# Optimization experiments

Hardware: AMD Instinct MI355X
Metric: run time of the kernel (lower is better)

## Reference

```python
import jax, jax.numpy as jnp
import numpy as np

N_NODES, N_EDGES, BATCH = 50000, 100000, 256
H = 64            # dim_hidden_features
D_NODE, D_EDGE, D_RBF = 110, 8, 8
D_SET = 2 * H     # Set2Set input_dim = 128, output_dim = 256
D_HID = 512
D_CAT = 54
MP_STEPS, S2S_ITERS = 4, 3


def setup_inputs() -> dict:
    key = jax.random.key(0)
    ks = iter(jax.random.split(key, 48))

    def nrm(shape, s=0.05):
        return jax.random.normal(next(ks), shape, dtype=jnp.float32) * s

    inp = {}
    inp["node_attribute"] = jax.random.normal(next(ks), (N_NODES, D_NODE), dtype=jnp.float32)
    inp["edge_attribute"] = jax.random.normal(next(ks), (N_EDGES, D_EDGE), dtype=jnp.float32)
    inp["edge_length"] = jax.random.uniform(next(ks), (N_EDGES,), dtype=jnp.float32)
    inp["src"] = jax.random.randint(next(ks), (N_EDGES,), 0, N_NODES, dtype=jnp.int32)
    inp["dst"] = jax.random.randint(next(ks), (N_EDGES,), 0, N_NODES, dtype=jnp.int32)
    inp["node_graph"] = jnp.sort(jax.random.randint(next(ks), (N_NODES,), 0, BATCH, dtype=jnp.int32))
    # atom_feature_projector
    inp["proj_W"] = nrm((D_NODE, H)); inp["proj_b"] = jnp.zeros((H,), jnp.float32)
    # RBF layer: centers ~ U(0,1), beta = 10 (per reset_parameters)
    inp["centers"] = jax.random.uniform(next(ks), (D_RBF,), dtype=jnp.float32)
    inp["beta"] = jnp.full((D_RBF,), 10.0, jnp.float32)
    # NNConv edge function: Linear(16 -> 64*64), plus NNConv bias
    inp["bond_W"] = nrm((D_EDGE + D_RBF, H * H)); inp["bond_b"] = jnp.zeros((H * H,), jnp.float32)
    inp["conv_b"] = jnp.zeros((H,), jnp.float32)
    # GRU (input H, hidden H); PyTorch layout (3H, in)
    inp["gru_Wih"] = nrm((3 * H, H)); inp["gru_Whh"] = nrm((3 * H, H))
    inp["gru_bih"] = jnp.zeros((3 * H,), jnp.float32); inp["gru_bhh"] = jnp.zeros((3 * H,), jnp.float32)
    # Set2Set LSTM: input 2*D_SET=256, hidden D_SET=128, 2 layers; PyTorch layout (4H, in)
    inp["lstm_Wih0"] = nrm((4 * D_SET, 2 * D_SET)); inp["lstm_Whh0"] = nrm((4 * D_SET, D_SET))
    inp["lstm_bih0"] = jnp.zeros((4 * D_SET,), jnp.float32); inp["lstm_bhh0"] = jnp.zeros((4 * D_SET,), jnp.float32)
    inp["lstm_Wih1"] = nrm((4 * D_SET, D_SET)); inp["lstm_Whh1"] = nrm((4 * D_SET, D_SET))
    inp["lstm_bih1"] = jnp.zeros((4 * D_SET,), jnp.float32); inp["lstm_bhh1"] = jnp.zeros((4 * D_SET,), jnp.float32)
    # sparsify: Linear(256 -> 512) + PReLU(init 0.25)
    inp["sp_W"] = nrm((2 * D_SET, D_HID)); inp["sp_b"] = jnp.zeros((D_HID,), jnp.float32)
    inp["prelu_a"] = jnp.array([0.25], jnp.float32)
    # catalyst1 head: hiddens[0] (512->512 ReLU, 512->512 Tanh) then outputs[0] (512->54)
    inp["h0_W1"] = nrm((D_HID, D_HID)); inp["h0_b1"] = jnp.zeros((D_HID,), jnp.float32)
    inp["h0_W2"] = nrm((D_HID, D_HID)); inp["h0_b2"] = jnp.zeros((D_HID,), jnp.float32)
    inp["out_W"] = nrm((D_HID, D_CAT)); inp["out_b"] = jnp.zeros((D_CAT,), jnp.float32)
    return inp


def _lstm_cell(x, h, c, Wih, Whh, bih, bhh):
    # PyTorch LSTM gate order: i, f, g, o
    g = x @ Wih.T + bih + h @ Whh.T + bhh
    i, f, gg, o = jnp.split(g, 4, axis=-1)
    c = jax.nn.sigmoid(f) * c + jax.nn.sigmoid(i) * jnp.tanh(gg)
    h = jax.nn.sigmoid(o) * jnp.tanh(c)
    return h, c


def reference(node_attribute, edge_attribute, edge_length, src, dst, node_graph,
              proj_W, proj_b, centers, beta, bond_W, bond_b, conv_b,
              gru_Wih, gru_Whh, gru_bih, gru_bhh,
              lstm_Wih0, lstm_Whh0, lstm_bih0, lstm_bhh0,
              lstm_Wih1, lstm_Whh1, lstm_bih1, lstm_bhh1,
              sp_W, sp_b, prelu_a, h0_W1, h0_b1, h0_W2, h0_b2, out_W, out_b):
    n_nodes = node_attribute.shape[0]
    # atom feature projection
    x = jax.nn.relu(node_attribute @ proj_W + proj_b)                       # (N, H)
    # edge features = [edge_attribute, RBF(length)]
    rbf = jnp.exp(-beta * (edge_length[:, None] - centers[None, :]) ** 2)   # (E, 8)
    efeat = jnp.concatenate([edge_attribute, rbf], axis=-1)                 # (E, 16)
    # NNConv per-edge weight matrix; edge features are constant over MP steps
    W_e = (efeat @ bond_W + bond_b).reshape(-1, H, H)                       # (E, H, H)

    feat, h = x, x
    for _ in range(MP_STEPS):
        # NNConv: message = h_src @ W_e, sum-aggregated at dst, plus bias
        m = jnp.einsum('ei,eio->eo', feat[src], W_e)                        # (E, H)
        agg = jax.ops.segment_sum(m, dst, num_segments=n_nodes) + conv_b    # (N, H)
        gx = jax.nn.relu(agg)
        # GRU cell (PyTorch gate order r, z, n)
        gi = gx @ gru_Wih.T + gru_bih
        gh = h @ gru_Whh.T + gru_bhh
        i_r, i_z, i_n = jnp.split(gi, 3, axis=-1)
        h_r, h_z, h_n = jnp.split(gh, 3, axis=-1)
        r = jax.nn.sigmoid(i_r + h_r)
        z = jax.nn.sigmoid(i_z + h_z)
        n = jnp.tanh(i_n + r * h_n)
        h = (1.0 - z) * n + z * h
        feat = h
    node_agg = jnp.concatenate([feat, x], axis=-1)                          # (N, 2H)

    # Set2Set pooling over graphs (segment softmax attention, 2-layer LSTM)
    B = BATCH
    h0 = c0 = jnp.zeros((B, D_SET), node_agg.dtype)
    h1 = c1 = jnp.zeros((B, D_SET), node_agg.dtype)
    q_star = jnp.zeros((B, 2 * D_SET), node_agg.dtype)
    for _ in range(S2S_ITERS):
        h0, c0 = _lstm_cell(q_star, h0, c0, lstm_Wih0, lstm_Whh0, lstm_bih0, lstm_bhh0)
        h1, c1 = _lstm_cell(h0, h1, c1, lstm_Wih1, lstm_Whh1, lstm_bih1, lstm_bhh1)
        q = h1                                                              # (B, 128)
        e = jnp.sum(node_agg * q[node_graph], axis=-1)                      # (N,)
        emax = jax.ops.segment_max(e, node_graph, num_segments=B)
        p = jnp.exp(e - emax[node_graph])
        denom = jax.ops.segment_sum(p, node_graph, num_segments=B)
        alpha = p / denom[node_graph]                                       # per-graph softmax
        r_out = jax.ops.segment_sum(node_agg * alpha[:, None], node_graph, num_segments=B)
        q_star = jnp.concatenate([q, r_out], axis=-1)                       # (B, 256)

    # sparsify (Linear + PReLU)
    feats = q_star @ sp_W + sp_b                                            # (B, 512)
    feats = jnp.where(feats >= 0, feats, prelu_a * feats)
    # catalyst1 head
    hid = jnp.tanh(jax.nn.relu(feats @ h0_W1 + h0_b1) @ h0_W2 + h0_b2)
    return jax.nn.softmax(hid @ out_W + out_b, axis=-1)                     # (B, 54)
```

## Files before the change

### kernel.cpp

```cpp
#include <hip/hip_runtime.h>
#include <math.h>

constexpr int N = 50000;
constexpr int E = 100000;
constexpr int B = 256;
constexpr int H = 64;
constexpr int DN = 110;
constexpr int NBLK = (E + 63) / 64;

#define DEV __device__ __forceinline__

typedef __attribute__((ext_vector_type(8))) short short8;
typedef __attribute__((ext_vector_type(4))) float floatx4;

DEV float sigf(float x) { return 1.0f / (1.0f + expf(-x)); }

DEV short f2bf(float f) {
    unsigned u = __float_as_uint(f);
    unsigned r = (u + 0x7fffu + ((u >> 16) & 1u)) >> 16;
    return (short)r;
}
DEV float bf2f(short s) { return __uint_as_float(((unsigned)(unsigned short)s) << 16); }

DEV void cvt8(const float* p, short8& hi, short8& lo) {
    float4 u0 = *(const float4*)p;
    float4 u1 = *(const float4*)(p + 4);
    float vv[8] = {u0.x, u0.y, u0.z, u0.w, u1.x, u1.y, u1.z, u1.w};
#pragma unroll
    for (int j = 0; j < 8; ++j) {
        short hb = f2bf(vv[j]);
        hi[j] = hb;
        lo[j] = f2bf(vv[j] - bf2f(hb));
    }
}

__global__ void k_izero(int* p, int n) {
    int i = blockIdx.x * 256 + threadIdx.x;
    if (i < n) p[i] = 0;
}

DEV void d_transpose(const float* in, float* out, int R, int C, int idx) {
    int r = idx / C, c = idx % C;
    out[c * R + r] = in[idx];
}

DEV void d_prepB(const float* __restrict__ W, short* __restrict__ out,
                 int NT16, int ld, int trans, int ocap, int kcap, int idx) {
    int lane = idx & 63;
    int t = idx >> 6;
    int ntile = t % NT16;
    int kt = t / NT16;
    int quad = lane >> 4, col = lane & 15;
    int o = ntile * 16 + col;
    short hi[8], lo[8];
#pragma unroll
    for (int j = 0; j < 8; ++j) {
        int k = kt * 32 + quad * 8 + j;
        float v = 0.0f;
        if (o < ocap && k < kcap) v = trans ? W[(size_t)o * ld + k] : W[(size_t)k * ld + o];
        short hb = f2bf(v);
        hi[j] = hb;
        lo[j] = f2bf(v - bf2f(hb));
    }
    short* dh = out + (((size_t)(t * 2 + 0) * 64 + lane) * 8);
    short* dl = out + (((size_t)(t * 2 + 1) * 64 + lane) * 8);
#pragma unroll
    for (int j = 0; j < 8; ++j) { dh[j] = hi[j]; dl[j] = lo[j]; }
}

DEV void d_prepW(const float* __restrict__ bond_W, const float* __restrict__ bond_b,
                 short* __restrict__ wf, int idx) {
    int lane = idx & 63;
    int t = idx >> 6;
    int ks = t & 1;
    int nt = (t >> 1) & 3;
    int kk = t >> 3;
    const float* S = (kk < 16) ? (bond_W + kk * 4096) : bond_b;
    int quad = lane >> 4, col = lane & 15;
    short hi[8], lo[8];
#pragma unroll
    for (int j = 0; j < 8; ++j) {
        int i = ks * 32 + quad * 8 + j;
        float v = S[i * 64 + nt * 16 + col];
        short hb = f2bf(v);
        hi[j] = hb;
        lo[j] = f2bf(v - bf2f(hb));
    }
    short* dh = wf + (((size_t)(t * 2 + 0) * 64 + lane) * 8);
    short* dl = wf + (((size_t)(t * 2 + 1) * 64 + lane) * 8);
#pragma unroll
    for (int j = 0; j < 8; ++j) { dh[j] = hi[j]; dl[j] = lo[j]; }
}

__launch_bounds__(256)
__global__ void k_prep0(const float* lWih0, const float* lWhh0, const float* lWih1, const float* lWhh1,
                        float* lW0T, float* lU0T, float* lW1T, float* lU1T,
                        const float* bond_W, const float* bond_b, short* wf,
                        const float* gru_Wih, const float* gru_Whh, short* fgI, short* fgH,
                        const float* proj_W, short* fproj,
                        float* zreg) {
    int idx = blockIdx.x * 256 + threadIdx.x;
    if (idx < 131072) { d_transpose(lWih0, lW0T, 512, 256, idx); return; }
    idx -= 131072;
    if (idx < 65536) { d_transpose(lWhh0, lU0T, 512, 128, idx); return; }
    idx -= 65536;
    if (idx < 65536) { d_transpose(lWih1, lW1T, 512, 128, idx); return; }
    idx -= 65536;
    if (idx < 65536) { d_transpose(lWhh1, lU1T, 512, 128, idx); return; }
    idx -= 65536;
    if (idx < 8704) { d_prepW(bond_W, bond_b, wf, idx); return; }
    idx -= 8704;
    if (idx < 1536) { d_prepB(gru_Wih, fgI, 12, 64, 1, 192, 64, idx); return; }
    idx -= 1536;
    if (idx < 1536) { d_prepB(gru_Whh, fgH, 12, 64, 1, 192, 64, idx); return; }
    idx -= 1536;
    if (idx < 1024) { d_prepB(proj_W, fproj, 4, 64, 0, 64, DN, idx); return; }
    idx -= 1024;
    if (idx < 196608) { zreg[idx] = 0.0f; return; }
}
constexpr int PREP0_TOTAL = 131072 + 3 * 65536 + 8704 + 2 * 1536 + 1024 + 196608;

__launch_bounds__(256)
__global__ void k_prephead(const float* sp_W, short* fsp, const float* h0_W1, short* fw1,
                           const float* h0_W2, short* fw2, const float* out_W, short* fow) {
    int idx = blockIdx.x * 256 + threadIdx.x;
    if (idx < 16384) { d_prepB(sp_W, fsp, 32, 512, 0, 512, 256, idx); return; }
    idx -= 16384;
    if (idx < 32768) { d_prepB(h0_W1, fw1, 32, 512, 0, 512, 512, idx); return; }
    idx -= 32768;
    if (idx < 32768) { d_prepB(h0_W2, fw2, 32, 512, 0, 512, 512, idx); return; }
    idx -= 32768;
    if (idx < 4096) { d_prepB(out_W, fow, 4, 54, 0, 54, 512, idx); return; }
}
constexpr int PREPH_TOTAL = 16384 + 2 * 32768 + 4096;

__global__ void k_deg(const int* __restrict__ dst, int* __restrict__ deg) {
    int e = blockIdx.x * 256 + threadIdx.x;
    if (e < E) atomicAdd(&deg[dst[e]], 1);
}
__global__ void k_scan1(const int* __restrict__ deg, int* __restrict__ bsum) {
    __shared__ int s[256];
    int b = blockIdx.x, tid = threadIdx.x;
    int idx = b * 256 + tid;
    s[tid] = (idx < N) ? deg[idx] : 0;
    __syncthreads();
    for (int st = 128; st > 0; st >>= 1) {
        if (tid < st) s[tid] += s[tid + st];
        __syncthreads();
    }
    if (tid == 0) bsum[b] = s[0];
}
__global__ void k_scan2p(int* __restrict__ bsum, int nb) {
    __shared__ int s[256];
    int tid = threadIdx.x;
    int v = (tid < nb) ? bsum[tid] : 0;
    s[tid] = v;
    __syncthreads();
    for (int off = 1; off < 256; off <<= 1) {
        int t = (tid >= off) ? s[tid - off] : 0;
        __syncthreads();
        s[tid] += t;
        __syncthreads();
    }
    if (tid < nb) bsum[tid] = s[tid] - v;
}
__global__ void k_scan3(const int* __restrict__ deg, const int* __restrict__ bsum,
                        int* __restrict__ cursor, int* __restrict__ roff) {
    __shared__ int s[256];
    int b = blockIdx.x, tid = threadIdx.x;
    int idx = b * 256 + tid;
    int v = (idx < N) ? deg[idx] : 0;
    s[tid] = v;
    __syncthreads();
    for (int off = 1; off < 256; off <<= 1) {
        int t = (tid >= off) ? s[tid - off] : 0;
        __syncthreads();
        s[tid] += t;
        __syncthreads();
    }
    if (idx < N) {
        int start = bsum[b] + s[tid] - v;
        cursor[idx] = start;
        roff[idx] = start;
    }
    if (idx == 0) roff[N] = E;
}
__global__ void k_scat(const int* __restrict__ src, const int* __restrict__ dst,
                       int* __restrict__ cursor, int* __restrict__ srcp,
                       int* __restrict__ epos, int* __restrict__ dstp) {
    int e = blockIdx.x * 256 + threadIdx.x;
    if (e >= E) return;
    int d = dst[e];
    int pos = atomicAdd(&cursor[d], 1);
    srcp[pos] = src[e];
    dstp[pos] = d;
    epos[e] = pos;
}

__launch_bounds__(256)
__global__ void k_projm(const float* __restrict__ na, const short* __restrict__ fp,
                        const float* __restrict__ b, float* __restrict__ x,
                        short* __restrict__ hs) {
    __shared__ float as[16 * 132];
    int tid = threadIdx.x, lane = tid & 63, nt = tid >> 6;
    int quad = lane >> 4, col = lane & 15;
    int s0 = blockIdx.x * 16;
    for (int i = tid; i < 16 * DN; i += 256) {
        int r = i / DN, c = i % DN;
        as[r * 132 + c] = na[(size_t)s0 * DN + i];
    }
    for (int i = tid; i < 16 * 22; i += 256) {
        int r = i / 22, c = DN + i % 22;
        as[r * 132 + c] = 0.0f;
    }
    __syncthreads();
    const short8* F = (const short8*)fp;
    floatx4 T = {0.0f, 0.0f, 0.0f, 0.0f};
#pragma unroll
    for (int kt = 0; kt < 4; ++kt) {
        const float* ap = as + col * 132 + kt * 32 + quad * 8;
        short8 ah, al;
#pragma unroll
        for (int j = 0; j < 8; ++j) {
            float v = ap[j];
            short hb = f2bf(v);
            ah[j] = hb;
            al[j] = f2bf(v - bf2f(hb));
        }
        int t = kt * 4 + nt;
        short8 bh = F[(t * 2 + 0) * 64 + lane];
        short8 bl = F[(t * 2 + 1) * 64 + lane];
        T = __builtin_amdgcn_mfma_f32_16x16x32_bf16(ah, bh, T, 0, 0, 0);
        T = __builtin_amdgcn_mfma_f32_16x16x32_bf16(al, bh, T, 0, 0, 0);
        T = __builtin_amdgcn_mfma_f32_16x16x32_bf16(ah, bl, T, 0, 0, 0);
    }
    int o = nt * 16 + col;
    float bo = b[o];
#pragma unroll
    for (int r = 0; r < 4; ++r) {
        int n = s0 + quad * 4 + r;
        float v = fmaxf(T[r] + bo, 0.0f);
        x[(size_t)n * 64 + o] = v;
        short hb = f2bf(v);
        hs[(size_t)n * 128 + o] = hb;
        hs[(size_t)n * 128 + 64 + o] = f2bf(v - bf2f(hb));
    }
}

__global__ void k_efeat2(const float* __restrict__ ea, const float* __restrict__ el,
                         const float* __restrict__ centers, const float* __restrict__ beta,
                         const int* __restrict__ epos, float* __restrict__ ef_t) {
    int e = blockIdx.x * 256 + threadIdx.x;
    if (e >= E) return;
    int pos = epos[e];
    float L = el[e];
#pragma unroll
    for (int j = 0; j < 8; ++j) ef_t[j * E + pos] = ea[e * 8 + j];
#pragma unroll
    for (int j = 0; j < 8; ++j) {
        float d = L - centers[j];
        ef_t[(8 + j) * E + pos] = expf(-beta[j] * d * d);
    }
    ef_t[16 * E + pos] = 1.0f;
}

__launch_bounds__(256)
__global__ void k_msgagg(const short* __restrict__ hs, const float* __restrict__ ef_t,
                         const short* __restrict__ wf, const int* __restrict__ srcp,
                         const int* __restrict__ dstp,
                         float* __restrict__ agg, float* __restrict__ bpart) {
    __shared__ float efs[17 * 64];
    __shared__ int srcs[64];
    __shared__ int dsh[64];
    __shared__ int shprev;
    __shared__ float Csh[64][65];

    int tid = threadIdx.x;
    int e0 = blockIdx.x * 64;
    int lane = tid & 63;
    int nt = tid >> 6;
    int quad = lane >> 4, col = lane & 15;

    if (tid < 64) {
        int eg = e0 + tid;
        srcs[tid] = (eg < E) ? srcp[eg] : 0;
        dsh[tid] = (eg < E) ? dstp[eg] : N;
    }
    if (tid == 0) shprev = (e0 == 0) ? -1 : dstp[e0 - 1];
    for (int i = tid; i < 17 * 64; i += 256) {
        int kk = i >> 6, e = i & 63;
        int eg = e0 + e;
        efs[i] = (eg < E) ? ef_t[(size_t)kk * E + eg] : 0.0f;
    }
    __syncthreads();

    short8 Ah[4][2], Al[4][2];
#pragma unroll
    for (int mt = 0; mt < 4; ++mt) {
        int s = srcs[mt * 16 + col];
        const short* hp = hs + (size_t)s * 128 + quad * 8;
#pragma unroll
        for (int ks = 0; ks < 2; ++ks) {
            Ah[mt][ks] = *(const short8*)(hp + ks * 32);
            Al[mt][ks] = *(const short8*)(hp + 64 + ks * 32);
        }
    }

    const short8* Wf = (const short8*)wf;
    float C[4][4] = {};

#define LOADB(d0, d1, d2, d3, KK)                      \
    {                                                  \
        int tb_ = ((KK) * 4 + nt) * 2;                 \
        d0 = Wf[((tb_ + 0) * 2 + 0) * 64 + lane];      \
        d1 = Wf[((tb_ + 1) * 2 + 0) * 64 + lane];      \
        d2 = Wf[((tb_ + 0) * 2 + 1) * 64 + lane];      \
        d3 = Wf[((tb_ + 1) * 2 + 1) * 64 + lane];      \
    }

    short8 c0, c1, c2, c3, n0_, n1_, n2_, n3_, q0, q1, q2, q3;
    LOADB(c0, c1, c2, c3, 0);
    LOADB(n0_, n1_, n2_, n3_, 1);
    LOADB(q0, q1, q2, q3, 2);

#pragma unroll 1
    for (int kk = 0; kk < 17; ++kk) {
        int kn = kk + 3;
        if (kn > 16) kn = 16;
        short8 p0, p1, p2, p3;
        LOADB(p0, p1, p2, p3, kn);

#pragma unroll
        for (int mt = 0; mt < 4; ++mt) {
            floatx4 T = {0.0f, 0.0f, 0.0f, 0.0f};
            T = __builtin_amdgcn_mfma_f32_16x16x32_bf16(Ah[mt][0], c0, T, 0, 0, 0);
            T = __builtin_amdgcn_mfma_f32_16x16x32_bf16(Ah[mt][1], c1, T, 0, 0, 0);
            T = __builtin_amdgcn_mfma_f32_16x16x32_bf16(Al[mt][0], c0, T, 0, 0, 0);
            T = __builtin_amdgcn_mfma_f32_16x16x32_bf16(Al[mt][1], c1, T, 0, 0, 0);
            T = __builtin_amdgcn_mfma_f32_16x16x32_bf16(Ah[mt][0], c2, T, 0, 0, 0);
            T = __builtin_amdgcn_mfma_f32_16x16x32_bf16(Ah[mt][1], c3, T, 0, 0, 0);
            float4 ef = *(const float4*)&efs[kk * 64 + mt * 16 + quad * 4];
            C[mt][0] += ef.x * T[0];
            C[mt][1] += ef.y * T[1];
            C[mt][2] += ef.z * T[2];
            C[mt][3] += ef.w * T[3];
        }
        c0 = n0_; c1 = n1_; c2 = n2_; c3 = n3_;
        n0_ = q0; n1_ = q1; n2_ = q2; n3_ = q3;
        q0 = p0; q1 = p1; q2 = p2; q3 = p3;
    }
#undef LOADB

#pragma unroll
    for (int mt = 0; mt < 4; ++mt)
#pragma unroll
        for (int r = 0; r < 4; ++r)
            Csh[mt * 16 + quad * 4 + r][nt * 16 + col] = C[mt][r];
    __syncthreads();

    if (tid < 64) {
        int c = tid;
        int prevd = shprev;
        int firstd = dsh[0];
        for (int q = prevd + 1; q < firstd; ++q) agg[(size_t)q * 64 + c] = 0.0f;
        int cur = firstd;
        float acc = 0.0f;
        bool owned = (e0 == 0) || (firstd != prevd);
        bool done = false;
        for (int r = 0; r < 64; ++r) {
            int d = dsh[r];
            if (d != cur) {
                if (owned) agg[(size_t)cur * 64 + c] = acc;
                else bpart[(size_t)blockIdx.x * 64 + c] = acc;
                int dc = (d < N) ? d : N;
                for (int q = cur + 1; q < dc; ++q) agg[(size_t)q * 64 + c] = 0.0f;
                cur = d;
                acc = 0.0f;
                owned = true;
                if (cur >= N) { done = true; break; }
            }
            acc += Csh[r][c];
        }
        if (!done) {
            if (owned) agg[(size_t)cur * 64 + c] = acc;
            else bpart[(size_t)blockIdx.x * 64 + c] = acc;
        }
    }
}

__launch_bounds__(256)
__global__ void k_gru4(const float* __restrict__ agg, const float* __restrict__ bpart,
                       const int* __restrict__ roff, const float* __restrict__ conv_b,
                       short* __restrict__ hs,
                       const short* __restrict__ fI, const short* __restrict__ fH,
                       const float* __restrict__ bih, const float* __restrict__ bhh) {
    int tid = threadIdx.x, lane = tid & 63, nt = tid >> 6;
    int quad = lane >> 4, col = lane & 15;
    int n0 = blockIdx.x * 32;

    short8 Gh[2][2], Gl[2][2], Hh[2][2], Hl[2][2];
#pragma unroll
    for (int mt = 0; mt < 2; ++mt) {
        int node = n0 + mt * 16 + col;
        bool ok = node < N;
        int nc = ok ? node : (N - 1);
        float acc[2][8];
        const float* ag = agg + (size_t)nc * 64;
#pragma unroll
        for (int ks = 0; ks < 2; ++ks) {
            const float* cb = conv_b + ks * 32 + quad * 8;
            float4 a0 = *(const float4*)(ag + ks * 32 + quad * 8);
            float4 a1 = *(const float4*)(ag + ks * 32 + quad * 8 + 4);
            acc[ks][0] = a0.x + cb[0]; acc[ks][1] = a0.y + cb[1];
            acc[ks][2] = a0.z + cb[2]; acc[ks][3] = a0.w + cb[3];
            acc[ks][4] = a1.x + cb[4]; acc[ks][5] = a1.y + cb[5];
            acc[ks][6] = a1.z + cb[6]; acc[ks][7] = a1.w + cb[7];
        }
        int rs = roff[nc];
        int re = roff[nc + 1];
        if (re > rs) {
            int b0 = rs >> 6, b1 = (re - 1) >> 6;
            for (int bb = b0 + 1; bb <= b1; ++bb) {
                const float* bp = bpart + (size_t)bb * 64;
#pragma unroll
                for (int ks = 0; ks < 2; ++ks) {
                    float4 p0 = *(const float4*)(bp + ks * 32 + quad * 8);
                    float4 p1 = *(const float4*)(bp + ks * 32 + quad * 8 + 4);
                    acc[ks][0] += p0.x; acc[ks][1] += p0.y;
                    acc[ks][2] += p0.z; acc[ks][3] += p0.w;
                    acc[ks][4] += p1.x; acc[ks][5] += p1.y;
                    acc[ks][6] += p1.z; acc[ks][7] += p1.w;
                }
            }
        }
        const short* hp = hs + (size_t)nc * 128 + quad * 8;
#pragma unroll
        for (int ks = 0; ks < 2; ++ks) {
            short8 hh8 = *(const short8*)(hp + ks * 32);
            short8 hl8 = *(const short8*)(hp + 64 + ks * 32);
            Hh[mt][ks] = hh8;
            Hl[mt][ks] = hl8;
#pragma unroll
            for (int j = 0; j < 8; ++j) {
                float g = ok ? fmaxf(acc[ks][j], 0.0f) : 0.0f;
                short gb = f2bf(g);
                Gh[mt][ks][j] = gb;
                Gl[mt][ks][j] = f2bf(g - bf2f(gb));
            }
        }
        if (!ok) {
#pragma unroll
            for (int ks = 0; ks < 2; ++ks) {
                Hh[mt][ks] = short8{0,0,0,0,0,0,0,0};
                Hl[mt][ks] = short8{0,0,0,0,0,0,0,0};
            }
        }
    }
    __syncthreads();

    const short8* FI = (const short8*)fI;
    const short8* FH = (const short8*)fH;
    floatx4 aI[2][3] = {}, aH[2][3] = {};
#pragma unroll
    for (int ks = 0; ks < 2; ++ks) {
        short8 bIh[3], bIl[3], bHh[3], bHl[3];
#pragma unroll
        for (int g = 0; g < 3; ++g) {
            int t = ks * 12 + g * 4 + nt;
            bIh[g] = FI[(t * 2 + 0) * 64 + lane];
            bIl[g] = FI[(t * 2 + 1) * 64 + lane];
            bHh[g] = FH[(t * 2 + 0) * 64 + lane];
            bHl[g] = FH[(t * 2 + 1) * 64 + lane];
        }
#pragma unroll
        for (int mt = 0; mt < 2; ++mt) {
#pragma unroll
            for (int g = 0; g < 3; ++g) {
                aI[mt][g] = __builtin_amdgcn_mfma_f32_16x16x32_bf16(Gh[mt][ks], bIh[g], aI[mt][g], 0, 0, 0);
                aI[mt][g] = __builtin_amdgcn_mfma_f32_16x16x32_bf16(Gl[mt][ks], bIh[g], aI[mt][g], 0, 0, 0);
                aI[mt][g] = __builtin_amdgcn_mfma_f32_16x16x32_bf16(Gh[mt][ks], bIl[g], aI[mt][g], 0, 0, 0);
                aH[mt][g] = __builtin_amdgcn_mfma_f32_16x16x32_bf16(Hh[mt][ks], bHh[g], aH[mt][g], 0, 0, 0);
                aH[mt][g] = __builtin_amdgcn_mfma_f32_16x16x32_bf16(Hl[mt][ks], bHh[g], aH[mt][g], 0, 0, 0);
                aH[mt][g] = __builtin_amdgcn_mfma_f32_16x16x32_bf16(Hh[mt][ks], bHl[g], aH[mt][g], 0, 0, 0);
            }
        }
    }

    int o = nt * 16 + col;
    float br = bih[o], bz = bih[64 + o], bn = bih[128 + o];
    float cr = bhh[o], cz = bhh[64 + o], cn = bhh[128 + o];
#pragma unroll
    for (int mt = 0; mt < 2; ++mt) {
#pragma unroll
        for (int r = 0; r < 4; ++r) {
            int node = n0 + mt * 16 + quad * 4 + r;
            if (node >= N) continue;
            float rg = sigf(aI[mt][0][r] + br + aH[mt][0][r] + cr);
            float z  = sigf(aI[mt][1][r] + bz + aH[mt][1][r] + cz);
            float ng = tanhf(aI[mt][2][r] + bn + rg * (aH[mt][2][r] + cn));
            size_t hb_ = (size_t)node * 128 + o;
            float hold = bf2f(hs[hb_]) + bf2f(hs[hb_ + 64]);
            float hn = (1.0f - z) * ng + z * hold;
            short hi = f2bf(hn);
            hs[hb_] = hi;
            hs[hb_ + 64] = f2bf(hn - bf2f(hi));
        }
    }
}

__global__ void k_bounds2(const int* __restrict__ ng, int* __restrict__ gs, int* __restrict__ ge) {
    int n = blockIdx.x * 256 + threadIdx.x;
    if (n >= N) return;
    int g = ng[n];
    int gp = (n == 0) ? -1 : ng[n - 1];
    if (g != gp) {
        gs[g] = n;
        if (n > 0) ge[gp] = n;
        for (int q = gp + 1; q < g; ++q) { gs[q] = 0; ge[q] = 0; }
    }
    if (n == N - 1) {
        ge[g] = N;
        for (int q = g + 1; q < B; ++q) { gs[q] = 0; ge[q] = 0; }
    }
}

__launch_bounds__(256)
__global__ void k_s2s(float* __restrict__ h0, float* __restrict__ c0,
                      float* __restrict__ h1, float* __restrict__ c1,
                      float* __restrict__ q_star,
                      const float* __restrict__ W0T, const float* __restrict__ U0T,
                      const float* __restrict__ b0i, const float* __restrict__ b0h,
                      const float* __restrict__ W1T, const float* __restrict__ U1T,
                      const float* __restrict__ b1i, const float* __restrict__ b1h,
                      const short* __restrict__ hs, const float* __restrict__ x,
                      const int* __restrict__ gs, const int* __restrict__ ge) {
    __shared__ float xb[256], hb[128], gb[512], h0n[128], qv[128];
    __shared__ float mrg[4][2][64];
    __shared__ float ml[4][2];
    int g = blockIdx.x, tid = threadIdx.x;
    xb[tid] = q_star[g * 256 + tid];
    if (tid < 128) hb[tid] = h0[g * 128 + tid];
    __syncthreads();
    float g0 = b0i[tid] + b0h[tid];
    float g1 = b0i[tid + 256] + b0h[tid + 256];
    for (int i = 0; i < 256; ++i) {
        float xx = xb[i];
        g0 += xx * W0T[i * 512 + tid];
        g1 += xx * W0T[i * 512 + tid + 256];
    }
    for (int i = 0; i < 128; ++i) {
        float hh = hb[i];
        g0 += hh * U0T[i * 512 + tid];
        g1 += hh * U0T[i * 512 + tid + 256];
    }
    gb[tid] = g0; gb[tid + 256] = g1;
    __syncthreads();
    if (tid < 128) {
        float ii = gb[tid], ff = gb[128 + tid], gg = gb[256 + tid], oo = gb[384 + tid];
        float c = sigf(ff) * c0[g * 128 + tid] + sigf(ii) * tanhf(gg);
        float hn = sigf(oo) * tanhf(c);
        c0[g * 128 + tid] = c; h0[g * 128 + tid] = hn; h0n[tid] = hn;
        hb[tid] = h1[g * 128 + tid];
    }
    __syncthreads();
    float ga = b1i[tid] + b1h[tid];
    float gbv = b1i[tid + 256] + b1h[tid + 256];
    for (int i = 0; i < 128; ++i) {
        float xx = h0n[i], hh = hb[i];
        ga  += xx * W1T[i * 512 + tid]       + hh * U1T[i * 512 + tid];
        gbv += xx * W1T[i * 512 + tid + 256] + hh * U1T[i * 512 + tid + 256];
    }
    gb[tid] = ga; gb[tid + 256] = gbv;
    __syncthreads();
    if (tid < 128) {
        float ii = gb[tid], ff = gb[128 + tid], gg = gb[256 + tid], oo = gb[384 + tid];
        float c = sigf(ff) * c1[g * 128 + tid] + sigf(ii) * tanhf(gg);
        float hn = sigf(oo) * tanhf(c);
        c1[g * 128 + tid] = c; h1[g * 128 + tid] = hn;
        q_star[g * 256 + tid] = hn;
        qv[tid] = hn;
    }
    __syncthreads();
    int s0v = gs[g], s1v = ge[g];
    int lane = tid & 63, grp = tid >> 6;
    float qh = qv[lane], qx = qv[64 + lane];
    float mM = -INFINITY, lL = 0.0f, nh = 0.0f, nx = 0.0f;
    for (int n = s0v + grp; n < s1v; n += 16) {
        float hv[4], xv[4], e[4];
#pragma unroll
        for (int j = 0; j < 4; ++j) {
            int nj = n + 4 * j;
            int nc = (nj < s1v) ? nj : n;
            hv[j] = bf2f(hs[(size_t)nc * 128 + lane]) + bf2f(hs[(size_t)nc * 128 + 64 + lane]);
            xv[j] = x[(size_t)nc * 64 + lane];
            e[j] = hv[j] * qh + xv[j] * qx;
        }
#pragma unroll
        for (int off = 32; off; off >>= 1) {
#pragma unroll
            for (int j = 0; j < 4; ++j) e[j] += __shfl_xor(e[j], off, 64);
        }
#pragma unroll
        for (int j = 0; j < 4; ++j)
            if (n + 4 * j >= s1v) e[j] = -INFINITY;
        float mb = fmaxf(fmaxf(e[0], e[1]), fmaxf(e[2], e[3]));
        float mn = fmaxf(mM, mb);
        float sc = expf(mM - mn);
        float w0 = expf(e[0] - mn), w1 = expf(e[1] - mn);
        float w2 = expf(e[2] - mn), w3 = expf(e[3] - mn);
        lL = lL * sc + ((w0 + w1) + (w2 + w3));
        nh = nh * sc + ((w0 * hv[0] + w1 * hv[1]) + (w2 * hv[2] + w3 * hv[3]));
        nx = nx * sc + ((w0 * xv[0] + w1 * xv[1]) + (w2 * xv[2] + w3 * xv[3]));
        mM = mn;
    }
    mrg[grp][0][lane] = nh;
    mrg[grp][1][lane] = nx;
    if (lane == 0) { ml[grp][0] = mM; ml[grp][1] = lL; }
    __syncthreads();
    if (tid < 128) {
        int half = tid >> 6, dl = tid & 63;
        float M = -INFINITY;
#pragma unroll
        for (int i = 0; i < 4; ++i) M = fmaxf(M, ml[i][0]);
        float L = 0.0f, NUM = 0.0f;
#pragma unroll
        for (int i = 0; i < 4; ++i) {
            float sc = expf(ml[i][0] - M);
            L += ml[i][1] * sc;
            NUM += mrg[i][half][dl] * sc;
        }
        q_star[g * 256 + 128 + tid] = (s1v > s0v) ? NUM / L : 0.0f;
    }
}

template<int MODE>
__launch_bounds__(256)
__global__ void k_hgemm(const float* __restrict__ A, const short* __restrict__ Bf,
                        const float* __restrict__ bias, const float* __restrict__ pa,
                        float* __restrict__ Cout, int K, int NT16) {
    int tid = threadIdx.x, lane = tid & 63, nt = tid >> 6;
    int quad = lane >> 4, col = lane & 15;
    int s0 = blockIdx.x * 16;
    int ntile = blockIdx.y * 4 + nt;
    int NoutTot = NT16 * 16;
    const short8* F = (const short8*)Bf;
    floatx4 T = {0.0f, 0.0f, 0.0f, 0.0f};
    const float* ap = A + (size_t)(s0 + col) * K + quad * 8;
    int KT = K >> 5;
#pragma unroll 4
    for (int kt = 0; kt < KT; ++kt) {
        short8 ah, al;
        cvt8(ap + kt * 32, ah, al);
        int t = kt * NT16 + ntile;
        short8 bh = F[(t * 2 + 0) * 64 + lane];
        short8 bl = F[(t * 2 + 1) * 64 + lane];
        T = __builtin_amdgcn_mfma_f32_16x16x32_bf16(ah, bh, T, 0, 0, 0);
        T = __builtin_amdgcn_mfma_f32_16x16x32_bf16(al, bh, T, 0, 0, 0);
        T = __builtin_amdgcn_mfma_f32_16x16x32_bf16(ah, bl, T, 0, 0, 0);
    }
    int o = ntile * 16 + col;
    float b = bias[o];
    float a = (MODE == 0) ? pa[0] : 0.0f;
#pragma unroll
    for (int r = 0; r < 4; ++r) {
        float v = T[r] + b;
        if (MODE == 0) v = (v >= 0.0f) ? v : a * v;
        if (MODE == 1) v = fmaxf(v, 0.0f);
        if (MODE == 2) v = tanhf(v);
        Cout[(size_t)(s0 + quad * 4 + r) * NoutTot + o] = v;
    }
}

__launch_bounds__(256)
__global__ void k_hout(const float* __restrict__ A, const short* __restrict__ Bf,
                       const float* __restrict__ ob, float* __restrict__ out) {
    __shared__ float sm[16][64];
    __shared__ float smax[16], sinv[16];
    int tid = threadIdx.x, lane = tid & 63, nt = tid >> 6;
    int quad = lane >> 4, col = lane & 15;
    int s0 = blockIdx.x * 16;
    const short8* F = (const short8*)Bf;
    floatx4 T = {0.0f, 0.0f, 0.0f, 0.0f};
    const float* ap = A + (size_t)(s0 + col) * 512 + quad * 8;
#pragma unroll 4
    for (int kt = 0; kt < 16; ++kt) {
        short8 ah, al;
        cvt8(ap + kt * 32, ah, al);
        int t = kt * 4 + nt;
        short8 bh = F[(t * 2 + 0) * 64 + lane];
        short8 bl = F[(t * 2 + 1) * 64 + lane];
        T = __builtin_amdgcn_mfma_f32_16x16x32_bf16(ah, bh, T, 0, 0, 0);
        T = __builtin_amdgcn_mfma_f32_16x16x32_bf16(al, bh, T, 0, 0, 0);
        T = __builtin_amdgcn_mfma_f32_16x16x32_bf16(ah, bl, T, 0, 0, 0);
    }
    int o = nt * 16 + col;
    float b = (o < 54) ? ob[o] : 0.0f;
#pragma unroll
    for (int r = 0; r < 4; ++r)
        sm[quad * 4 + r][o] = (o < 54) ? (T[r] + b) : -1e30f;
    __syncthreads();
    if (tid < 16) {
        float m = -INFINITY;
        for (int j = 0; j < 54; ++j) m = fmaxf(m, sm[tid][j]);
        float s = 0.0f;
        for (int j = 0; j < 54; ++j) s += expf(sm[tid][j] - m);
        smax[tid] = m;
        sinv[tid] = 1.0f / s;
    }
    __syncthreads();
    for (int idx = tid; idx < 16 * 54; idx += 256) {
        int srow = idx / 54, oo = idx % 54;
        out[(size_t)(s0 + srow) * 54 + oo] = expf(sm[srow][oo] - smax[srow]) * sinv[srow];
    }
}

extern "C" void kernel_launch(void* const* d_in, const int* in_sizes, int n_in,
                              void* d_out, int out_size, void* d_ws, size_t ws_size,
                              hipStream_t stream) {
    const float* node_attr = (const float*)d_in[0];
    const float* edge_attr = (const float*)d_in[1];
    const float* edge_len  = (const float*)d_in[2];
    const int*   src       = (const int*)d_in[3];
    const int*   dst       = (const int*)d_in[4];
    const int*   node_grph = (const int*)d_in[5];
    const float* proj_W    = (const float*)d_in[6];
    const float* proj_b    = (const float*)d_in[7];
    const float* centers   = (const float*)d_in[8];
    const float* beta      = (const float*)d_in[9];
    const float* bond_W    = (const float*)d_in[10];
    const float* bond_b    = (const float*)d_in[11];
    const float* conv_b    = (const float*)d_in[12];
    const float* gru_Wih   = (const float*)d_in[13];
    const float* gru_Whh   = (const float*)d_in[14];
    const float* gru_bih   = (const float*)d_in[15];
    const float* gru_bhh   = (const float*)d_in[16];
    const float* lWih0     = (const float*)d_in[17];
    const float* lWhh0     = (const float*)d_in[18];
    const float* lbih0     = (const float*)d_in[19];
    const float* lbhh0     = (const float*)d_in[20];
    const float* lWih1     = (const float*)d_in[21];
    const float* lWhh1     = (const float*)d_in[22];
    const float* lbih1     = (const float*)d_in[23];
    const float* lbhh1     = (const float*)d_in[24];
    const float* sp_W      = (const float*)d_in[25];
    const float* sp_b      = (const float*)d_in[26];
    const float* prelu_a   = (const float*)d_in[27];
    const float* h0_W1     = (const float*)d_in[28];
    const float* h0_b1     = (const float*)d_in[29];
    const float* h0_W2     = (const float*)d_in[30];
    const float* h0_b2     = (const float*)d_in[31];
    const float* out_W     = (const float*)d_in[32];
    const float* out_b     = (const float*)d_in[33];
    float* out = (float*)d_out;

    float* ws = (float*)d_ws;
    size_t off = 0;
    float* x      = ws + off; off += (size_t)N * 64;
    float* hsf    = ws + off; off += (size_t)N * 64;
    float* ef_t   = ws + off; off += (size_t)E * 17;
    float* agg    = ws + off; off += (size_t)N * 64;
    float* wfrag  = ws + off; off += 17 * 16 * 64 * 8 / 2;
    float* fgI    = ws + off; off += 2 * 64 * 192 / 2;
    float* fgH    = ws + off; off += 2 * 64 * 192 / 2;
    float* fproj  = ws + off; off += 16 * 1024 / 2;
    float* lW0T   = ws + off; off += 256 * 512;
    float* lU0T   = ws + off; off += 128 * 512;
    float* lW1T   = ws + off; off += 128 * 512;
    float* lU1T   = ws + off; off += 128 * 512;
    float* h0     = ws + off; off += B * 128;
    float* c0     = ws + off; off += B * 128;
    float* h1     = ws + off; off += B * 128;
    float* c1     = ws + off; off += B * 128;
    float* q_star = ws + off; off += B * 256;
    float* bpart  = ws + off; off += (size_t)NBLK * 64;
    int* gs       = (int*)(ws + off); off += B;
    int* ge       = (int*)(ws + off); off += B;
    int* deg      = (int*)(ws + off); off += N;
    int* cursor   = (int*)(ws + off); off += N;
    int* roff     = (int*)(ws + off); off += N + 1;
    int* bsum     = (int*)(ws + off); off += 256;
    int* srcp     = (int*)(ws + off); off += E;
    int* epos     = (int*)(ws + off); off += E;
    int* dstp     = (int*)(ws + off); off += E;

    short* hs = (short*)hsf;

    short* fsp = (short*)ef_t;
    short* fw1 = (short*)(ef_t + 131072);
    short* fw2 = (short*)(ef_t + 131072 + 262144);
    short* fow = (short*)(ef_t + 131072 + 2 * 262144);
    float* hb1 = ef_t + 131072 + 2 * 262144 + 32768;
    float* hb2 = hb1 + 131072;

    constexpr int NB = (N + 255) / 256;

    k_izero<<<NB, 256, 0, stream>>>(deg, N);
    k_deg<<<(E + 255) / 256, 256, 0, stream>>>(dst, deg);
    k_scan1<<<NB, 256, 0, stream>>>(deg, bsum);
    k_scan2p<<<1, 256, 0, stream>>>(bsum, NB);
    k_scan3<<<NB, 256, 0, stream>>>(deg, bsum, cursor, roff);
    k_scat<<<(E + 255) / 256, 256, 0, stream>>>(src, dst, cursor, srcp, epos, dstp);

    k_prep0<<<(PREP0_TOTAL + 255) / 256, 256, 0, stream>>>(
        lWih0, lWhh0, lWih1, lWhh1, lW0T, lU0T, lW1T, lU1T,
        bond_W, bond_b, (short*)wfrag, gru_Wih, gru_Whh, (short*)fgI, (short*)fgH,
        proj_W, (short*)fproj, h0);

    k_projm<<<N / 16, 256, 0, stream>>>(node_attr, (const short*)fproj, proj_b, x, hs);
    k_efeat2<<<(E + 255) / 256, 256, 0, stream>>>(edge_attr, edge_len, centers, beta, epos, ef_t);

    k_bounds2<<<(N + 255) / 256, 256, 0, stream>>>(node_grph, gs, ge);

    for (int step = 0; step < 4; ++step) {
        k_msgagg<<<NBLK, 256, 0, stream>>>(hs, ef_t, (const short*)wfrag, srcp, dstp,
                                           agg, bpart);
        k_gru4<<<(N + 31) / 32, 256, 0, stream>>>(agg, bpart, roff, conv_b, hs,
                                                  (const short*)fgI, (const short*)fgH,
                                                  gru_bih, gru_bhh);
    }

    k_prephead<<<(PREPH_TOTAL + 255) / 256, 256, 0, stream>>>(
        sp_W, fsp, h0_W1, fw1, h0_W2, fw2, out_W, fow);

    for (int it = 0; it < 3; ++it) {
        k_s2s<<<B, 256, 0, stream>>>(h0, c0, h1, c1, q_star,
                                     lW0T, lU0T, lbih0, lbhh0,
                                     lW1T, lU1T, lbih1, lbhh1,
                                     hs, x, gs, ge);
    }

    k_hgemm<0><<<dim3(16, 8), 256, 0, stream>>>(q_star, fsp, sp_b, prelu_a, hb1, 256, 32);
    k_hgemm<1><<<dim3(16, 8), 256, 0, stream>>>(hb1, fw1, h0_b1, nullptr, hb2, 512, 32);
    k_hgemm<2><<<dim3(16, 8), 256, 0, stream>>>(hb2, fw2, h0_b2, nullptr, hb1, 512, 32);
    k_hout<<<16, 256, 0, stream>>>(hb1, fow, out_b, out);
}
```

Before: 734.7 us.

## Fuse edge-feature and graph-bounds prep into prep0, pack LSTM weights as pairs

Moves the edge-feature and graph-boundary computations into the existing prep0 kernel, which removes two launches. LSTM weights are repacked so that each thread reads a float2 holding its two gate columns instead of two strided loads. On the last GRU step the kernel also writes fp32 hidden state into the agg buffer, so Set2Set reads one float instead of rebuilding it from two bf16 halves. The Csh padding changes from 65 to 68, and agg loses __restrict__ because it is reused as the output. The in-place reuse of agg is a risk if another block of the same GRU launch still reads those rows.

Result: faster. 701.7 us (-4.5%).

```diff
diff --git a/kernel.cpp b/kernel.cpp
--- a/kernel.cpp
+++ b/kernel.cpp
@@ -39,9 +39,11 @@
     if (i < n) p[i] = 0;
 }
 
-DEV void d_transpose(const float* in, float* out, int R, int C, int idx) {
-    int r = idx / C, c = idx % C;
-    out[c * R + r] = in[idx];
+DEV void d_packpair(const float* __restrict__ in, float* __restrict__ out, int IN_I, int idx) {
+    int i = idx >> 8;
+    int j = idx & 255;
+    out[2 * idx]     = in[(size_t)j * IN_I + i];
+    out[2 * idx + 1] = in[(size_t)(j + 256) * IN_I + i];
 }
 
 DEV void d_prepB(const float* __restrict__ W, short* __restrict__ out,
@@ -94,20 +96,23 @@
 
 __launch_bounds__(256)
 __global__ void k_prep0(const float* lWih0, const float* lWhh0, const float* lWih1, const float* lWhh1,
-                        float* lW0T, float* lU0T, float* lW1T, float* lU1T,
+                        float* lW0P, float* lU0P, float* lW1P, float* lU1P,
                         const float* bond_W, const float* bond_b, short* wf,
                         const float* gru_Wih, const float* gru_Whh, short* fgI, short* fgH,
                         const float* proj_W, short* fproj,
+                        const float* ea, const float* el, const float* centers,
+                        const float* beta, const int* epos, float* ef_t,
+                        const int* ng, int* gs, int* ge,
                         float* zreg) {
     int idx = blockIdx.x * 256 + threadIdx.x;
-    if (idx < 131072) { d_transpose(lWih0, lW0T, 512, 256, idx); return; }
-    idx -= 131072;
-    if (idx < 65536) { d_transpose(lWhh0, lU0T, 512, 128, idx); return; }
+    if (idx < 65536) { d_packpair(lWih0, lW0P, 256, idx); return; }
     idx -= 65536;
-    if (idx < 65536) { d_transpose(lWih1, lW1T, 512, 128, idx); return; }
-    idx -= 65536;
-    if (idx < 65536) { d_transpose(lWhh1, lU1T, 512, 128, idx); return; }
-    idx -= 65536;
+    if (idx < 32768) { d_packpair(lWhh0, lU0P, 128, idx); return; }
+    idx -= 32768;
+    if (idx < 32768) { d_packpair(lWih1, lW1P, 128, idx); return; }
+    idx -= 32768;
+    if (idx < 32768) { d_packpair(lWhh1, lU1P, 128, idx); return; }
+    idx -= 32768;
     if (idx < 8704) { d_prepW(bond_W, bond_b, wf, idx); return; }
     idx -= 8704;
     if (idx < 1536) { d_prepB(gru_Wih, fgI, 12, 64, 1, 192, 64, idx); return; }
@@ -116,9 +121,40 @@
     idx -= 1536;
     if (idx < 1024) { d_prepB(proj_W, fproj, 4, 64, 0, 64, DN, idx); return; }
     idx -= 1024;
+    if (idx < E) {
+        int e = idx;
+        int pos = epos[e];
+        float L = el[e];
+#pragma unroll
+        for (int j = 0; j < 8; ++j) ef_t[(size_t)j * E + pos] = ea[e * 8 + j];
+#pragma unroll
+        for (int j = 0; j < 8; ++j) {
+            float d = L - centers[j];
+            ef_t[(size_t)(8 + j) * E + pos] = expf(-beta[j] * d * d);
+        }
+        ef_t[(size_t)16 * E + pos] = 1.0f;
+        return;
+    }
+    idx -= E;
+    if (idx < N) {
+        int n = idx;
+        int g = ng[n];
+        int gp = (n == 0) ? -1 : ng[n - 1];
+        if (g != gp) {
+            gs[g] = n;
+            if (n > 0) ge[gp] = n;
+            for (int q = gp + 1; q < g; ++q) { gs[q] = 0; ge[q] = 0; }
+        }
+        if (n == N - 1) {
+            ge[g] = N;
+            for (int q = g + 1; q < B; ++q) { gs[q] = 0; ge[q] = 0; }
+        }
+        return;
+    }
+    idx -= N;
     if (idx < 196608) { zreg[idx] = 0.0f; return; }
 }
-constexpr int PREP0_TOTAL = 131072 + 3 * 65536 + 8704 + 2 * 1536 + 1024 + 196608;
+constexpr int PREP0_TOTAL = 65536 + 3 * 32768 + 8704 + 2 * 1536 + 1024 + E + N + 196608;
 
 __launch_bounds__(256)
 __global__ void k_prephead(const float* sp_W, short* fsp, const float* h0_W1, short* fw1,
@@ -247,23 +283,6 @@
     }
 }
 
-__global__ void k_efeat2(const float* __restrict__ ea, const float* __restrict__ el,
-                         const float* __restrict__ centers, const float* __restrict__ beta,
-                         const int* __restrict__ epos, float* __restrict__ ef_t) {
-    int e = blockIdx.x * 256 + threadIdx.x;
-    if (e >= E) return;
-    int pos = epos[e];
-    float L = el[e];
-#pragma unroll
-    for (int j = 0; j < 8; ++j) ef_t[j * E + pos] = ea[e * 8 + j];
-#pragma unroll
-    for (int j = 0; j < 8; ++j) {
-        float d = L - centers[j];
-        ef_t[(8 + j) * E + pos] = expf(-beta[j] * d * d);
-    }
-    ef_t[16 * E + pos] = 1.0f;
-}
-
 __launch_bounds__(256)
 __global__ void k_msgagg(const short* __restrict__ hs, const float* __restrict__ ef_t,
                          const short* __restrict__ wf, const int* __restrict__ srcp,
@@ -273,7 +292,7 @@
     __shared__ int srcs[64];
     __shared__ int dsh[64];
     __shared__ int shprev;
-    __shared__ float Csh[64][65];
+    __shared__ float Csh[64][68];
 
     int tid = threadIdx.x;
     int e0 = blockIdx.x * 64;
@@ -389,11 +408,12 @@
 }
 
 __launch_bounds__(256)
-__global__ void k_gru4(const float* __restrict__ agg, const float* __restrict__ bpart,
+__global__ void k_gru4(const float* agg, const float* __restrict__ bpart,
                        const int* __restrict__ roff, const float* __restrict__ conv_b,
                        short* __restrict__ hs,
                        const short* __restrict__ fI, const short* __restrict__ fH,
-                       const float* __restrict__ bih, const float* __restrict__ bhh) {
+                       const float* __restrict__ bih, const float* __restrict__ bhh,
+                       float* hf) {
     int tid = threadIdx.x, lane = tid & 63, nt = tid >> 6;
     int quad = lane >> 4, col = lane & 15;
     int n0 = blockIdx.x * 32;
@@ -504,23 +524,8 @@
             short hi = f2bf(hn);
             hs[hb_] = hi;
             hs[hb_ + 64] = f2bf(hn - bf2f(hi));
-        }
-    }
-}
-
-__global__ void k_bounds2(const int* __restrict__ ng, int* __restrict__ gs, int* __restrict__ ge) {
-    int n = blockIdx.x * 256 + threadIdx.x;
-    if (n >= N) return;
-    int g = ng[n];
-    int gp = (n == 0) ? -1 : ng[n - 1];
-    if (g != gp) {
-        gs[g] = n;
-        if (n > 0) ge[gp] = n;
-        for (int q = gp + 1; q < g; ++q) { gs[q] = 0; ge[q] = 0; }
-    }
-    if (n == N - 1) {
-        ge[g] = N;
-        for (int q = g + 1; q < B; ++q) { gs[q] = 0; ge[q] = 0; }
+            if (hf) hf[(size_t)node * 64 + o] = hn;
+        }
     }
 }
 
@@ -528,11 +533,11 @@
 __global__ void k_s2s(float* __restrict__ h0, float* __restrict__ c0,
                       float* __restrict__ h1, float* __restrict__ c1,
                       float* __restrict__ q_star,
-                      const float* __restrict__ W0T, const float* __restrict__ U0T,
+                      const float* __restrict__ W0P, const float* __restrict__ U0P,
                       const float* __restrict__ b0i, const float* __restrict__ b0h,
-                      const float* __restrict__ W1T, const float* __restrict__ U1T,
+                      const float* __restrict__ W1P, const float* __restrict__ U1P,
                       const float* __restrict__ b1i, const float* __restrict__ b1h,
-                      const short* __restrict__ hs, const float* __restrict__ x,
+                      const float* __restrict__ hf, const float* __restrict__ x,
                       const int* __restrict__ gs, const int* __restrict__ ge) {
     __shared__ float xb[256], hb[128], gb[512], h0n[128], qv[128];
     __shared__ float mrg[4][2][64];
@@ -545,13 +550,15 @@
     float g1 = b0i[tid + 256] + b0h[tid + 256];
     for (int i = 0; i < 256; ++i) {
         float xx = xb[i];
-        g0 += xx * W0T[i * 512 + tid];
-        g1 += xx * W0T[i * 512 + tid + 256];
+        float2 w = *(const float2*)(W0P + 2 * (i * 256 + tid));
+        g0 += xx * w.x;
+        g1 += xx * w.y;
     }
     for (int i = 0; i < 128; ++i) {
         float hh = hb[i];
-        g0 += hh * U0T[i * 512 + tid];
-        g1 += hh * U0T[i * 512 + tid + 256];
+        float2 w = *(const float2*)(U0P + 2 * (i * 256 + tid));
+        g0 += hh * w.x;
+        g1 += hh * w.y;
     }
     gb[tid] = g0; gb[tid + 256] = g1;
     __syncthreads();
@@ -567,8 +574,10 @@
     float gbv = b1i[tid + 256] + b1h[tid + 256];
     for (int i = 0; i < 128; ++i) {
         float xx = h0n[i], hh = hb[i];
-        ga  += xx * W1T[i * 512 + tid]       + hh * U1T[i * 512 + tid];
-        gbv += xx * W1T[i * 512 + tid + 256] + hh * U1T[i * 512 + tid + 256];
+        float2 w1 = *(const float2*)(W1P + 2 * (i * 256 + tid));
+        float2 u1 = *(const float2*)(U1P + 2 * (i * 256 + tid));
+        ga  += xx * w1.x + hh * u1.x;
+        gbv += xx * w1.y + hh * u1.y;
     }
     gb[tid] = ga; gb[tid + 256] = gbv;
     __syncthreads();
@@ -591,7 +600,7 @@
         for (int j = 0; j < 4; ++j) {
             int nj = n + 4 * j;
             int nc = (nj < s1v) ? nj : n;
-            hv[j] = bf2f(hs[(size_t)nc * 128 + lane]) + bf2f(hs[(size_t)nc * 128 + 64 + lane]);
+            hv[j] = hf[(size_t)nc * 64 + lane];
             xv[j] = x[(size_t)nc * 64 + lane];
             e[j] = hv[j] * qh + xv[j] * qx;
         }
@@ -763,10 +772,10 @@
     float* fgI    = ws + off; off += 2 * 64 * 192 / 2;
     float* fgH    = ws + off; off += 2 * 64 * 192 / 2;
     float* fproj  = ws + off; off += 16 * 1024 / 2;
-    float* lW0T   = ws + off; off += 256 * 512;
-    float* lU0T   = ws + off; off += 128 * 512;
-    float* lW1T   = ws + off; off += 128 * 512;
-    float* lU1T   = ws + off; off += 128 * 512;
+    float* lW0P   = ws + off; off += 256 * 512;
+    float* lU0P   = ws + off; off += 128 * 512;
+    float* lW1P   = ws + off; off += 128 * 512;
+    float* lU1P   = ws + off; off += 128 * 512;
     float* h0     = ws + off; off += B * 128;
     float* c0     = ws + off; off += B * 128;
     float* h1     = ws + off; off += B * 128;
@@ -802,21 +811,21 @@
     k_scat<<<(E + 255) / 256, 256, 0, stream>>>(src, dst, cursor, srcp, epos, dstp);
 
     k_prep0<<<(PREP0_TOTAL + 255) / 256, 256, 0, stream>>>(
-        lWih0, lWhh0, lWih1, lWhh1, lW0T, lU0T, lW1T, lU1T,
+        lWih0, lWhh0, lWih1, lWhh1, lW0P, lU0P, lW1P, lU1P,
         bond_W, bond_b, (short*)wfrag, gru_Wih, gru_Whh, (short*)fgI, (short*)fgH,
-        proj_W, (short*)fproj, h0);
+        proj_W, (short*)fproj,
+        edge_attr, edge_len, centers, beta, epos, ef_t,
+        node_grph, gs, ge, h0);
 
     k_projm<<<N / 16, 256, 0, stream>>>(node_attr, (const short*)fproj, proj_b, x, hs);
-    k_efeat2<<<(E + 255) / 256, 256, 0, stream>>>(edge_attr, edge_len, centers, beta, epos, ef_t);
-
-    k_bounds2<<<(N + 255) / 256, 256, 0, stream>>>(node_grph, gs, ge);
 
     for (int step = 0; step < 4; ++step) {
         k_msgagg<<<NBLK, 256, 0, stream>>>(hs, ef_t, (const short*)wfrag, srcp, dstp,
                                            agg, bpart);
         k_gru4<<<(N + 31) / 32, 256, 0, stream>>>(agg, bpart, roff, conv_b, hs,
                                                   (const short*)fgI, (const short*)fgH,
-                                                  gru_bih, gru_bhh);
+                                                  gru_bih, gru_bhh,
+                                                  (step == 3) ? agg : nullptr);
     }
 
     k_prephead<<<(PREPH_TOTAL + 255) / 256, 256, 0, stream>>>(
@@ -824,9 +833,9 @@
 
     for (int it = 0; it < 3; ++it) {
         k_s2s<<<B, 256, 0, stream>>>(h0, c0, h1, c1, q_star,
-                                     lW0T, lU0T, lbih0, lbhh0,
-                                     lW1T, lU1T, lbih1, lbhh1,
-                                     hs, x, gs, ge);
+                                     lW0P, lU0P, lbih0, lbhh0,
+                                     lW1P, lU1P, lbih1, lbhh1,
+                                     agg, x, gs, ge);
     }
 
     k_hgemm<0><<<dim3(16, 8), 256, 0, stream>>>(q_star, fsp, sp_b, prelu_a, hb1, 256, 32);
```
